# Kernel optimization log

Hardware: AMD Instinct MI355X
Metric: run time of the kernel (lower is better)

Reference implementation:

```python
import jax, jax.numpy as jnp
import numpy as np

D_HEAD = 128


def setup_inputs() -> dict:
    key = jax.random.key(0)
    k1, k2, k3 = jax.random.split(key, 3)
    batch, num_q, seq_len, d = 16, 64, 4096, D_HEAD
    query = jax.random.normal(k1, (batch, num_q, d), dtype=jnp.float32)
    keys = jax.random.normal(k2, (batch, seq_len, d), dtype=jnp.float32)
    values = jax.random.normal(k3, (batch, seq_len, d), dtype=jnp.float32)
    return {"query": query, "keys": keys, "values": values}


def reference(query, keys, values):
    # AttentionJacobian.forward with 3D query -> compute_attention_jacobian_batched
    # J[b,q] = scale * ( sum_n a[b,q,n] v[b,n] k[b,n]^T  -  (a V)[b,q] ((a K)[b,q])^T )
    d_k = keys.shape[-1]
    scale = d_k ** (-0.5)
    scores = jnp.einsum('bqd,bnd->bqn', query, keys) * scale
    attn_weights = jax.nn.softmax(scores, axis=-1)            # (b, q, n)
    attn_outputs = jnp.einsum('bqn,bnv->bqv', attn_weights, values)
    # term1 without materializing (b, q, n, v, k): fuse as single contraction
    term1 = jnp.einsum('bqn,bnv,bnk->bqvk', attn_weights, values, keys)
    weighted_keys_sum = jnp.einsum('bqn,bnk->bqk', attn_weights, keys)
    term2 = jnp.einsum('bqv,bqk->bqvk', attn_outputs, weighted_keys_sum)
    jacobians = scale * (term1 - term2)                       # (b, q, d_v, d_k)
    return jacobians
```

## Files before the change

### kernel.cpp

```cpp
#include <hip/hip_runtime.h>
#include <stdint.h>

typedef _Float16 f16;
typedef _Float16 half4 __attribute__((ext_vector_type(4)));
typedef _Float16 half8 __attribute__((ext_vector_type(8)));
typedef float f32x4 __attribute__((ext_vector_type(4)));

#define BATCH 16
#define NQ 64
#define SL 4096
#define DH 128


__global__ __launch_bounds__(256) void kprep(const float* __restrict__ Kg,
                                             const float* __restrict__ Vg,
                                             f16* __restrict__ Kt,
                                             f16* __restrict__ Vt) {
  __shared__ f16 Ld[128][130];
  const int blk = blockIdx.x;
  const int b = blk >> 6;
  const int tensor = (blk >> 5) & 1;
  const int chunk = blk & 31;
  const float* src = tensor ? Vg : Kg;
  f16* dst = tensor ? Vt : Kt;
  const int t = threadIdx.x;
  const int n0 = chunk * 128;
  {
    const int d = t & 127;
    const int nl = t >> 7;
    const float* s = src + ((size_t)b * SL + n0 + nl) * DH + d;
    for (int it = 0; it < 64; ++it)
      Ld[d][nl + it * 2] = (f16)s[(size_t)it * 2 * DH];
  }
  __syncthreads();
  {
    const int r = t & 15;
    const int kc = (t >> 4) & 3;
    const int w = t >> 6;
    char* dstb = (char*)(dst + (size_t)b * DH * SL);
#pragma unroll
    for (int tl = 0; tl < 4; ++tl)
#pragma unroll
      for (int hh = 0; hh < 2; ++hh) {
        const int dhi = w + hh * 4;
        const int d = dhi * 16 + r;
        const int nl = tl * 32 + kc * 8;
        const half8 v = *(const half8*)&Ld[d][nl];
        *(half8*)(dstb + (size_t)(chunk * 4 + tl) * 8192 + dhi * 1024 +
                  kc * 256 + r * 16) = v;
      }
  }
}

__global__ __launch_bounds__(256) void kscore(const float* __restrict__ Q,
                                              const f16* __restrict__ Kt,
                                              f16* __restrict__ E,
                                              float* __restrict__ denomp) {
  const int blk = (blockIdx.x & 7) * 64 + (blockIdx.x >> 3);
  __shared__ float Qs[8][128];
  __shared__ float wsum[4][4];
  const int b = blk >> 5;
  const int qg = (blk >> 2) & 7;
  const int ns = blk & 3;
  const int t = threadIdx.x;
  for (int i = t; i < 8 * 128; i += 256)
    Qs[i >> 7][i & 127] = Q[((size_t)b * NQ + qg * 8 + (i >> 7)) * DH + (i & 127)];
  __syncthreads();
  const int w = t >> 6, l = t & 63;
  const int q0 = (w >> 1) * 4;
  const int nbase = ns * 1024 + (w & 1) * 512 + l * 8;
  const f16* kb = Kt + (size_t)b * DH * SL + (size_t)(nbase >> 5) * 4096 +
                  (size_t)((nbase >> 3) & 3) * 128;
  float acc[4][8] = {};
  for (int d = 0; d < DH; ++d) {
    const half8 kv = *(const half8*)(kb + (d >> 4) * 512 + (d & 15) * 8);
    float kf[8];
#pragma unroll
    for (int j = 0; j < 8; ++j) kf[j] = (float)kv[j];
#pragma unroll
    for (int qi = 0; qi < 4; ++qi) {
      const float qv = Qs[q0 + qi][d];
#pragma unroll
      for (int j = 0; j < 8; ++j) acc[qi][j] += qv * kf[j];
    }
  }
  const float scl = 0.08838834764831845f;
#pragma unroll
  for (int qi = 0; qi < 4; ++qi) {
    half8 ev;
    float ds = 0.f;
#pragma unroll
    for (int j = 0; j < 8; ++j) {
      ev[j] = (f16)__expf(acc[qi][j] * scl);
      ds += (float)ev[j];
    }
    *(half8*)&E[((size_t)b * NQ + qg * 8 + q0 + qi) * SL + nbase] = ev;
    for (int off = 1; off < 64; off <<= 1) ds += __shfl_xor(ds, off);
    if (l == 0) wsum[w][qi] = ds;
  }
  __syncthreads();
  if (t < 8) {
    const int hw = (t >> 2) * 2;
    denomp[(size_t)ns * BATCH * NQ + (size_t)b * NQ + qg * 8 + t] =
        wsum[hw][t & 3] + wsum[hw + 1][t & 3];
  }
}

__global__ __launch_bounds__(256) void kev(const f16* __restrict__ Vt,
                                           const f16* __restrict__ Kt,
                                           const f16* __restrict__ E,
                                           float* __restrict__ EVp,
                                           float* __restrict__ EKp) {
  __shared__ __align__(16) f16 Es[32][40];
  const int blk = (blockIdx.x & 7) * 32 + (blockIdx.x >> 3);
  const int b = blk >> 4;
  const int tensor = (blk >> 3) & 1;
  const int nq = (blk >> 1) & 3;
  const int qh = blk & 1;
  const char* src = (const char*)((tensor ? Kt : Vt) + (size_t)b * DH * SL);
  float* dst = (tensor ? EKp : EVp) +
               ((size_t)nq * BATCH * NQ + (size_t)b * NQ + qh * 32) * DH;
  const f16* Eb = E + ((size_t)b * NQ + qh * 32) * SL + nq * 1024;
  const int t = threadIdx.x, w = t >> 6, l = t & 63;
  const int eq = t >> 3;
  const int en = (t & 7) * 4;

  f32x4 acc[2][2] = {};

  for (int chunk = 0; chunk < 32; ++chunk) {
    *(half4*)&Es[eq][en] = *(const half4*)(Eb + (size_t)eq * SL + chunk * 32 + en);
    __syncthreads();
    const int n0 = nq * 1024 + chunk * 32;
    const size_t gb = (size_t)(n0 >> 5) * 8192 + l * 16;
    const half8 a0 = *(const half8*)(src + gb + w * 1024);
    const half8 a1 = *(const half8*)(src + gb + (w + 4) * 1024);
    half8 b0, b1;
#pragma unroll
    for (int j = 0; j < 8; ++j) {
      b0[j] = Es[l & 15][(l >> 4) * 8 + j];
      b1[j] = Es[16 + (l & 15)][(l >> 4) * 8 + j];
    }
    acc[0][0] = __builtin_amdgcn_mfma_f32_16x16x32_f16(a0, b0, acc[0][0], 0, 0, 0);
    acc[0][1] = __builtin_amdgcn_mfma_f32_16x16x32_f16(a0, b1, acc[0][1], 0, 0, 0);
    acc[1][0] = __builtin_amdgcn_mfma_f32_16x16x32_f16(a1, b0, acc[1][0], 0, 0, 0);
    acc[1][1] = __builtin_amdgcn_mfma_f32_16x16x32_f16(a1, b1, acc[1][1], 0, 0, 0);
    __syncthreads();
  }

#pragma unroll
  for (int sv2 = 0; sv2 < 2; ++sv2)
#pragma unroll
    for (int qsub = 0; qsub < 2; ++qsub) {
      const int q = qsub * 16 + (l & 15);
      const int row = (w + sv2 * 4) * 16 + (l >> 4) * 4;
      *(f32x4*)&dst[(size_t)q * DH + row] = acc[sv2][qsub];
    }
}

__global__ __launch_bounds__(512, 2) void kjac(
    const f16* __restrict__ Vt, const f16* __restrict__ Kt,
    const f16* __restrict__ E, const float* __restrict__ EV,
    const float* __restrict__ EK, const float* __restrict__ denomp,
    float* __restrict__ out) {
  __shared__ __align__(16) f16 El[4][4096];
  const int blk = (blockIdx.x & 7) * 32 + (blockIdx.x >> 3);
  const int b = blk >> 4;
  const int q0 = (blk & 15) * 4;
  const int t = threadIdx.x, w = t >> 6, l = t & 63;
  const int sA = (w >> 2) * 4;
  const int sB = (w & 3) * 2;
  const char* vtb = (const char*)(Vt + (size_t)b * DH * SL) + sA * 1024 + l * 16;
  const char* ktb = (const char*)(Kt + (size_t)b * DH * SL) + sB * 1024 + l * 16;

  {
    const f16* Eg = E + ((size_t)b * NQ + q0) * SL;
#pragma unroll
    for (int p = 0; p < 4; ++p)
      *(half8*)&El[p][t * 8] = *(const half8*)(Eg + (size_t)p * SL + t * 8);
  }
  __syncthreads();

  f32x4 acc[4][4][2] = {};
  half8 vfA[4], kfA[2], efA[4], vfB[4], kfB[2], efB[4];
  const int eoff = (l >> 4) * 8;

#define LOADF(vf, kf, ef, tile)                                              \
  {                                                                          \
    const size_t gb = (size_t)(tile) * 8192;                                 \
    _Pragma("unroll") for (int i = 0; i < 4; ++i) vf[i] =                    \
        *(const half8*)(vtb + gb + i * 1024);                                \
    _Pragma("unroll") for (int j = 0; j < 2; ++j) kf[j] =                    \
        *(const half8*)(ktb + gb + j * 1024);                                \
    _Pragma("unroll") for (int q = 0; q < 4; ++q) ef[q] =                    \
        *(const half8*)&El[q][(tile) * 32 + eoff];                           \
  }

#define MFMA32(vf, kf, ef)                                                   \
  {                                                                          \
    __builtin_amdgcn_s_setprio(1);                                           \
    _Pragma("unroll") for (int q = 0; q < 4; ++q) {                          \
      const half8 uk0 = ef[q] * kf[0];                                       \
      const half8 uk1 = ef[q] * kf[1];                                       \
      _Pragma("unroll") for (int i = 0; i < 4; ++i) {                        \
        acc[q][i][0] = __builtin_amdgcn_mfma_f32_16x16x32_f16(               \
            vf[i], uk0, acc[q][i][0], 0, 0, 0);                              \
        acc[q][i][1] = __builtin_amdgcn_mfma_f32_16x16x32_f16(               \
            vf[i], uk1, acc[q][i][1], 0, 0, 0);                              \
      }                                                                      \
    }                                                                        \
    __builtin_amdgcn_s_setprio(0);                                           \
  }

  LOADF(vfA, kfA, efA, 0)
  for (int tt = 0; tt < 126; tt += 2) {
    LOADF(vfB, kfB, efB, tt + 1)
    MFMA32(vfA, kfA, efA)
    LOADF(vfA, kfA, efA, tt + 2)
    MFMA32(vfB, kfB, efB)
  }
  LOADF(vfB, kfB, efB, 127)
  MFMA32(vfA, kfA, efA)
  MFMA32(vfB, kfB, efB)
#undef LOADF
#undef MFMA32

  const float scl = 0.08838834764831845f;
  const size_t PS = (size_t)BATCH * NQ * DH;
  const size_t DS = (size_t)BATCH * NQ;
#pragma unroll
  for (int q = 0; q < 4; ++q) {
    const size_t qi = (size_t)b * NQ + q0 + q;
    float den = 0.f;
#pragma unroll
    for (int p = 0; p < 4; ++p) den += denomp[p * DS + qi];
    const float invd = 1.0f / den;
    const float* evq = EV + qi * DH;
    const float* ekq = EK + qi * DH;
    float* ob = out + qi * DH * DH;
#pragma unroll
    for (int i = 0; i < 4; ++i) {
      const int row0 = (sA + i) * 16 + (l >> 4) * 4;
      f32x4 ev4 = *(const f32x4*)&evq[row0];
#pragma unroll
      for (int p = 1; p < 4; ++p) ev4 += *(const f32x4*)&evq[p * PS + row0];
#pragma unroll
      for (int j = 0; j < 2; ++j) {
        const int col = (sB + j) * 16 + (l & 15);
        float ek = ekq[col];
#pragma unroll
        for (int p = 1; p < 4; ++p) ek += ekq[p * PS + col];
#pragma unroll
        for (int r = 0; r < 4; ++r)
          ob[(size_t)(row0 + r) * DH + col] =
              scl * invd * (acc[q][i][j][r] - invd * ev4[r] * ek);
      }
    }
  }
}

extern "C" void kernel_launch(void* const* d_in, const int* in_sizes, int n_in,
                              void* d_out, int out_size, void* d_ws,
                              size_t ws_size, hipStream_t stream) {
  const float* Q = (const float*)d_in[0];
  const float* K = (const float*)d_in[1];
  const float* V = (const float*)d_in[2];
  float* out = (float*)d_out;

  f16* Vt = (f16*)d_ws;
  f16* Kt = Vt + (size_t)BATCH * DH * SL;
  f16* Ef = Kt + (size_t)BATCH * DH * SL;
  float* EVp = (float*)(Ef + (size_t)BATCH * NQ * SL);
  float* EKp = EVp + 4 * (size_t)BATCH * NQ * DH;
  float* denomp = EKp + 4 * (size_t)BATCH * NQ * DH;

  kprep<<<1024, 256, 0, stream>>>(K, V, Kt, Vt);
  kscore<<<512, 256, 0, stream>>>(Q, Kt, Ef, denomp);
  kev<<<256, 256, 0, stream>>>(Vt, Kt, Ef, EVp, EKp);
  kjac<<<256, 512, 0, stream>>>(Vt, Kt, Ef, EVp, EKp, denomp, out);
}
```

Measured before the change: 176.4 us.

## Fuse EV and EK products in kev and stage larger E tiles

The kev kernel now computes the E·V and E·K partial products in the same block, so each staged tile of E in shared memory is reused for both. Blocks now split the sequence into 8 partitions instead of 4 and stage 128 columns per sync instead of 32, which means fewer barriers and wider, vectorised LDS reads. The cost is more accumulator registers, twice as many partial buffers, and 8-way partial sums read back in kjac.

```diff
diff --git a/kernel.cpp b/kernel.cpp
--- a/kernel.cpp
+++ b/kernel.cpp
@@ -111,49 +111,59 @@
                                            const f16* __restrict__ E,
                                            float* __restrict__ EVp,
                                            float* __restrict__ EKp) {
-  __shared__ __align__(16) f16 Es[32][40];
+  __shared__ __align__(16) f16 Es[32][136];
   const int blk = (blockIdx.x & 7) * 32 + (blockIdx.x >> 3);
   const int b = blk >> 4;
-  const int tensor = (blk >> 3) & 1;
-  const int nq = (blk >> 1) & 3;
+  const int ne = (blk >> 1) & 7;
   const int qh = blk & 1;
-  const char* src = (const char*)((tensor ? Kt : Vt) + (size_t)b * DH * SL);
-  float* dst = (tensor ? EKp : EVp) +
-               ((size_t)nq * BATCH * NQ + (size_t)b * NQ + qh * 32) * DH;
-  const f16* Eb = E + ((size_t)b * NQ + qh * 32) * SL + nq * 1024;
+  const char* vsrc = (const char*)(Vt + (size_t)b * DH * SL);
+  const char* ksrc = (const char*)(Kt + (size_t)b * DH * SL);
+  const f16* Eb = E + ((size_t)b * NQ + qh * 32) * SL + ne * 512;
   const int t = threadIdx.x, w = t >> 6, l = t & 63;
   const int eq = t >> 3;
-  const int en = (t & 7) * 4;
-
-  f32x4 acc[2][2] = {};
-
-  for (int chunk = 0; chunk < 32; ++chunk) {
-    *(half4*)&Es[eq][en] = *(const half4*)(Eb + (size_t)eq * SL + chunk * 32 + en);
+  const int en = (t & 7) * 16;
+
+  f32x4 accV[2][2] = {}, accK[2][2] = {};
+
+  for (int sc = 0; sc < 4; ++sc) {
     __syncthreads();
-    const int n0 = nq * 1024 + chunk * 32;
-    const size_t gb = (size_t)(n0 >> 5) * 8192 + l * 16;
-    const half8 a0 = *(const half8*)(src + gb + w * 1024);
-    const half8 a1 = *(const half8*)(src + gb + (w + 4) * 1024);
-    half8 b0, b1;
-#pragma unroll
-    for (int j = 0; j < 8; ++j) {
-      b0[j] = Es[l & 15][(l >> 4) * 8 + j];
-      b1[j] = Es[16 + (l & 15)][(l >> 4) * 8 + j];
-    }
-    acc[0][0] = __builtin_amdgcn_mfma_f32_16x16x32_f16(a0, b0, acc[0][0], 0, 0, 0);
-    acc[0][1] = __builtin_amdgcn_mfma_f32_16x16x32_f16(a0, b1, acc[0][1], 0, 0, 0);
-    acc[1][0] = __builtin_amdgcn_mfma_f32_16x16x32_f16(a1, b0, acc[1][0], 0, 0, 0);
-    acc[1][1] = __builtin_amdgcn_mfma_f32_16x16x32_f16(a1, b1, acc[1][1], 0, 0, 0);
+    {
+      const f16* ep = Eb + (size_t)eq * SL + sc * 128 + en;
+      *(half8*)&Es[eq][en] = *(const half8*)ep;
+      *(half8*)&Es[eq][en + 8] = *(const half8*)(ep + 8);
+    }
     __syncthreads();
-  }
-
+    const int nbase = ne * 512 + sc * 128;
+#pragma unroll
+    for (int c = 0; c < 4; ++c) {
+      const size_t gb = (size_t)((nbase + c * 32) >> 5) * 8192 + l * 16;
+      const half8 b0 = *(const half8*)&Es[l & 15][c * 32 + (l >> 4) * 8];
+      const half8 b1 = *(const half8*)&Es[16 + (l & 15)][c * 32 + (l >> 4) * 8];
+      const half8 av0 = *(const half8*)(vsrc + gb + w * 1024);
+      const half8 av1 = *(const half8*)(vsrc + gb + (w + 4) * 1024);
+      const half8 ak0 = *(const half8*)(ksrc + gb + w * 1024);
+      const half8 ak1 = *(const half8*)(ksrc + gb + (w + 4) * 1024);
+      accV[0][0] = __builtin_amdgcn_mfma_f32_16x16x32_f16(av0, b0, accV[0][0], 0, 0, 0);
+      accV[0][1] = __builtin_amdgcn_mfma_f32_16x16x32_f16(av0, b1, accV[0][1], 0, 0, 0);
+      accV[1][0] = __builtin_amdgcn_mfma_f32_16x16x32_f16(av1, b0, accV[1][0], 0, 0, 0);
+      accV[1][1] = __builtin_amdgcn_mfma_f32_16x16x32_f16(av1, b1, accV[1][1], 0, 0, 0);
+      accK[0][0] = __builtin_amdgcn_mfma_f32_16x16x32_f16(ak0, b0, accK[0][0], 0, 0, 0);
+      accK[0][1] = __builtin_amdgcn_mfma_f32_16x16x32_f16(ak0, b1, accK[0][1], 0, 0, 0);
+      accK[1][0] = __builtin_amdgcn_mfma_f32_16x16x32_f16(ak1, b0, accK[1][0], 0, 0, 0);
+      accK[1][1] = __builtin_amdgcn_mfma_f32_16x16x32_f16(ak1, b1, accK[1][1], 0, 0, 0);
+    }
+  }
+
+  float* dstV = EVp + ((size_t)ne * BATCH * NQ + (size_t)b * NQ + qh * 32) * DH;
+  float* dstK = EKp + ((size_t)ne * BATCH * NQ + (size_t)b * NQ + qh * 32) * DH;
 #pragma unroll
   for (int sv2 = 0; sv2 < 2; ++sv2)
 #pragma unroll
     for (int qsub = 0; qsub < 2; ++qsub) {
       const int q = qsub * 16 + (l & 15);
       const int row = (w + sv2 * 4) * 16 + (l >> 4) * 4;
-      *(f32x4*)&dst[(size_t)q * DH + row] = acc[sv2][qsub];
+      *(f32x4*)&dstV[(size_t)q * DH + row] = accV[sv2][qsub];
+      *(f32x4*)&dstK[(size_t)q * DH + row] = accK[sv2][qsub];
     }
 }
 
@@ -242,13 +252,13 @@
       const int row0 = (sA + i) * 16 + (l >> 4) * 4;
       f32x4 ev4 = *(const f32x4*)&evq[row0];
 #pragma unroll
-      for (int p = 1; p < 4; ++p) ev4 += *(const f32x4*)&evq[p * PS + row0];
+      for (int p = 1; p < 8; ++p) ev4 += *(const f32x4*)&evq[p * PS + row0];
 #pragma unroll
       for (int j = 0; j < 2; ++j) {
         const int col = (sB + j) * 16 + (l & 15);
         float ek = ekq[col];
 #pragma unroll
-        for (int p = 1; p < 4; ++p) ek += ekq[p * PS + col];
+        for (int p = 1; p < 8; ++p) ek += ekq[p * PS + col];
 #pragma unroll
         for (int r = 0; r < 4; ++r)
           ob[(size_t)(row0 + r) * DH + col] =
@@ -270,8 +280,8 @@
   f16* Kt = Vt + (size_t)BATCH * DH * SL;
   f16* Ef = Kt + (size_t)BATCH * DH * SL;
   float* EVp = (float*)(Ef + (size_t)BATCH * NQ * SL);
-  float* EKp = EVp + 4 * (size_t)BATCH * NQ * DH;
-  float* denomp = EKp + 4 * (size_t)BATCH * NQ * DH;
+  float* EKp = EVp + 8 * (size_t)BATCH * NQ * DH;
+  float* denomp = EKp + 8 * (size_t)BATCH * NQ * DH;
 
   kprep<<<1024, 256, 0, stream>>>(K, V, Kt, Vt);
   kscore<<<512, 256, 0, stream>>>(Q, Kt, Ef, denomp);
```

After: 176.9 us. Within noise of the previous version (+0.3%).
